# Optimization experiments

Measured on AMD Instinct MI355X. Metric: run time of the kernel, lower is better.

Reference implementation:

```python
import jax, jax.numpy as jnp
import numpy as np

B, T, D_MODEL, HEAD_DIM = 4, 4096, 2048, 128
NEG = -1e9  # matches torch's -1000000000.0 mask fill


def setup_inputs() -> dict:
    key = jax.random.key(0)
    ks = jax.random.split(key, 7)
    s = 0.02
    return {
        "x": jax.random.normal(ks[0], (B, T, D_MODEL), dtype=jnp.float32),
        "q_w": jax.random.normal(ks[1], (HEAD_DIM, D_MODEL), dtype=jnp.float32) * s,
        "q_b": jax.random.normal(ks[2], (HEAD_DIM,), dtype=jnp.float32) * s,
        "k_w": jax.random.normal(ks[3], (HEAD_DIM, D_MODEL), dtype=jnp.float32) * s,
        "k_b": jax.random.normal(ks[4], (HEAD_DIM,), dtype=jnp.float32) * s,
        "v_w": jax.random.normal(ks[5], (HEAD_DIM, D_MODEL), dtype=jnp.float32) * s,
        "v_b": jax.random.normal(ks[6], (HEAD_DIM,), dtype=jnp.float32) * s,
    }


def reference(x, q_w, q_b, k_w, k_b, v_w, v_b):
    # Linear projections: y = x @ W^T + b  -> [B, T, head_dim]
    q = jnp.einsum("btc,hc->bth", x, q_w) + q_b
    k = jnp.einsum("btc,hc->bth", x, k_w) + k_b
    v = jnp.einsum("btc,hc->bth", x, v_w) + v_b

    head_dim = q.shape[-1]
    # scores [B, T, T], scaled by 1/sqrt(head_dim)
    scores = jnp.einsum("bqh,bkh->bqk", q, k) / jnp.sqrt(jnp.float32(head_dim))
    # causal mask: additive -1e9 above the diagonal (future positions)
    t = scores.shape[-1]
    mask = jnp.triu(jnp.full((t, t), NEG, dtype=scores.dtype), k=1)
    scores = scores + mask
    probs = jax.nn.softmax(scores, axis=-1)
    # dropout p=0.0 -> identity (eval)
    y = jnp.einsum("bqk,bkh->bqh", probs, v)
    return y
```

## Files before the change

### kernel.cpp

```cpp
#include <hip/hip_runtime.h>

#define T_SEQ 4096
#define DMODEL 2048
#define HD 128

typedef float f32x4 __attribute__((ext_vector_type(4)));
typedef _Float16 f16x8 __attribute__((ext_vector_type(8)));

__device__ __forceinline__ unsigned short f2h(float f) {
  union { _Float16 h; unsigned short u; } v;
  v.h = (_Float16)f;
  return v.u;
}

__device__ __forceinline__ unsigned pk2h(float lo, float hi) {
  return (unsigned)f2h(lo) | ((unsigned)f2h(hi) << 16);
}

template <int CTRL>
__device__ __forceinline__ float dppmax(float x) {
  union { float f; int i; } a, b;
  a.f = x;
  b.i = __builtin_amdgcn_update_dpp(a.i, a.i, CTRL, 0xF, 0xF, false);
  return fmaxf(x, b.f);
}
template <int CTRL>
__device__ __forceinline__ float dppadd(float x) {
  union { float f; int i; } a, b;
  a.f = x;
  b.i = __builtin_amdgcn_update_dpp(a.i, a.i, CTRL, 0xF, 0xF, false);
  return x + b.f;
}
__device__ __forceinline__ float red16_max(float x) {
  x = dppmax<0xB1>(x); x = dppmax<0x4E>(x);
  x = dppmax<0x124>(x); x = dppmax<0x128>(x);
  return x;
}
__device__ __forceinline__ float red16_add(float x) {
  x = dppadd<0xB1>(x); x = dppadd<0x4E>(x);
  x = dppadd<0x124>(x); x = dppadd<0x128>(x);
  return x;
}

__global__ __launch_bounds__(256) void cvt_w_kernel(
    const float* __restrict__ qw, const float* __restrict__ qb,
    const float* __restrict__ kw, const float* __restrict__ kb,
    const float* __restrict__ vw, const float* __restrict__ vb,
    unsigned short* __restrict__ wb, float* __restrict__ biasc) {
  int idx = blockIdx.x * 256 + threadIdx.x;
  int e = idx * 4;
  int row = e >> 11;
  int col = e & 2047;
  const float* src = (row < 128) ? (qw + row * 2048)
                   : (row < 256) ? (kw + (row - 128) * 2048)
                                 : (vw + (row - 256) * 2048);
  float4 v = *(const float4*)(src + col);
  ushort4 o;
  o.x = f2h(v.x); o.y = f2h(v.y); o.z = f2h(v.z); o.w = f2h(v.w);
  *(ushort4*)(wb + e) = o;
  if (blockIdx.x == 0 && threadIdx.x < 384) {
    int n = threadIdx.x;
    biasc[n] = (n < 128) ? qb[n] : (n < 256) ? kb[n - 128] : vb[n - 256];
  }
}

#define SAB 40
__global__ __launch_bounds__(256, 3) void proj_kernel(
    const float* __restrict__ x, const unsigned short* __restrict__ wb,
    const float* __restrict__ biasc, unsigned short* __restrict__ qkv) {
  __shared__ unsigned short sA[64 * SAB];
  __shared__ unsigned short sB[128 * SAB];
  const int tid = threadIdx.x;
  const int lane = tid & 63;
  const int w = tid >> 6;
  const int fr = lane & 15;
  const int g = lane >> 4;
  const int m0 = blockIdx.x * 64;
  const int n0 = blockIdx.y * 128;
  const int wm = (w & 1) * 32;
  const int wn = (w >> 1) * 64;

  const int arow = tid >> 2;
  const int acolA = (tid & 3) * 8;
  const int brow = tid >> 1;
  const int bcolB = (tid & 1) * 16;
  const float* xp = x + (size_t)(m0 + arow) * DMODEL + acolA;
  const unsigned short* bp = wb + (size_t)(n0 + brow) * DMODEL + bcolB;

  f32x4 acc[2][4] = {};
  float4 ax0 = *(const float4*)(xp);
  float4 ax1 = *(const float4*)(xp + 4);
  uint4 bx0 = *(const uint4*)(bp);
  uint4 bx1 = *(const uint4*)(bp + 8);

  for (int k0 = 0; k0 < DMODEL; k0 += 32) {
    __syncthreads();
    uint4 pa;
    pa.x = pk2h(ax0.x, ax0.y); pa.y = pk2h(ax0.z, ax0.w);
    pa.z = pk2h(ax1.x, ax1.y); pa.w = pk2h(ax1.z, ax1.w);
    *(uint4*)&sA[arow * SAB + acolA] = pa;
    *(uint4*)&sB[brow * SAB + bcolB] = bx0;
    *(uint4*)&sB[brow * SAB + bcolB + 8] = bx1;
    __syncthreads();

    if (k0 + 32 < DMODEL) {
      ax0 = *(const float4*)(xp + k0 + 32);
      ax1 = *(const float4*)(xp + k0 + 36);
      bx0 = *(const uint4*)(bp + k0 + 32);
      bx1 = *(const uint4*)(bp + k0 + 40);
    }

    f16x8 af[2], bf[4];
#pragma unroll
    for (int i = 0; i < 2; ++i)
      af[i] = *(const f16x8*)&sA[(wm + 16 * i + fr) * SAB + g * 8];
#pragma unroll
    for (int jn = 0; jn < 4; ++jn)
      bf[jn] = *(const f16x8*)&sB[(wn + 16 * jn + fr) * SAB + g * 8];
#pragma unroll
    for (int i = 0; i < 2; ++i)
#pragma unroll
      for (int jn = 0; jn < 4; ++jn)
        acc[i][jn] = __builtin_amdgcn_mfma_f32_16x16x32_f16(af[i], bf[jn], acc[i][jn], 0, 0, 0);
  }

#pragma unroll
  for (int jn = 0; jn < 4; ++jn) {
    int n = n0 + wn + 16 * jn + fr;
    float bias = biasc[n];
#pragma unroll
    for (int i = 0; i < 2; ++i) {
      int mb = m0 + wm + 16 * i + g * 4;
#pragma unroll
      for (int r = 0; r < 4; ++r)
        qkv[(size_t)(mb + r) * 384 + n] = f2h(acc[i][jn][r] + bias);
    }
  }
}

#define SKS 136
#define SVS 72
#define SPS 72
__global__ __launch_bounds__(256, 3) void attn_kernel(
    const unsigned short* __restrict__ qkv, float* __restrict__ out,
    float* __restrict__ po, float* __restrict__ pml, int split) {
  __shared__ unsigned short sK[64 * SKS];
  __shared__ unsigned short sVt[128 * SVS];
  __shared__ unsigned short sP[64 * SPS];
  const int id = blockIdx.x;
  const int batch = blockIdx.y;
  int qt, c, nc;
  if (split) {
    if (id < 16)      { qt = id;                c = 0;          nc = 1; }
    else if (id < 48) { qt = 16 + ((id - 16) >> 1); c = (id - 16) & 1; nc = 2; }
    else if (id < 96) { qt = 32 + (id - 48) / 3;    c = (id - 48) % 3; nc = 3; }
    else              { qt = 48 + ((id - 96) >> 2); c = (id - 96) & 3; nc = 4; }
  } else { qt = id; c = 0; nc = 1; }
  const int qbase = qt * 64;
  const int t0 = c * 16;
  const int tend = min(t0 + 16, qt + 1);
  const int tid = threadIdx.x;
  const int lane = tid & 63;
  const int w = tid >> 6;
  const int fr = lane & 15;
  const int g = lane >> 4;
  const int va = tid >> 4;
  const int vu = tid & 15;
  const int vblk = ((va ^ (vu & 14)) << 2);
  const unsigned short* qkvb = qkv + (size_t)batch * T_SEQ * 384;

  f16x8 qf[4];
  {
    const unsigned short* qp = qkvb + (size_t)(qbase + 16 * w + fr) * 384 + g * 8;
#pragma unroll
    for (int s = 0; s < 4; ++s) qf[s] = *(const f16x8*)(qp + 32 * s);
  }
  f32x4 o[8] = {};
  float m_r[4], l_r[4];
#pragma unroll
  for (int r = 0; r < 4; ++r) { m_r[r] = -1e30f; l_r[r] = 0.f; }
  const float scale = 0.08838834764831845f;

  uint4 pk[4], pvv[4];
#pragma unroll
  for (int it = 0; it < 4; ++it) {
    int idx = it * 256 + tid;
    pk[it] = *(const uint4*)(qkvb + (size_t)(t0 * 64 + (idx >> 4)) * 384 + 128 + (idx & 15) * 8);
  }
#pragma unroll
  for (int i = 0; i < 4; ++i)
    pvv[i] = *(const uint4*)(qkvb + (size_t)(t0 * 64 + va + 16 * i) * 384 + 256 + vu * 8);

  for (int t = t0; t < tend; ++t) {
    const int kbase = t * 64;
    __syncthreads();
#pragma unroll
    for (int it = 0; it < 4; ++it) {
      int idx = it * 256 + tid;
      *(uint4*)&sK[(idx >> 4) * SKS + (idx & 15) * 8] = pk[it];
    }
    {
      const unsigned* w0 = (const unsigned*)&pvv[0];
      const unsigned* w1 = (const unsigned*)&pvv[1];
      const unsigned* w2 = (const unsigned*)&pvv[2];
      const unsigned* w3 = (const unsigned*)&pvv[3];
#pragma unroll
      for (int j2 = 0; j2 < 4; ++j2) {
        uint2 se, so;
        se.x = __builtin_amdgcn_perm(w1[j2], w0[j2], 0x05040100);
        se.y = __builtin_amdgcn_perm(w3[j2], w2[j2], 0x05040100);
        so.x = __builtin_amdgcn_perm(w1[j2], w0[j2], 0x07060302);
        so.y = __builtin_amdgcn_perm(w3[j2], w2[j2], 0x07060302);
        *(uint2*)&sVt[(8 * vu + 2 * j2) * SVS + vblk] = se;
        *(uint2*)&sVt[(8 * vu + 2 * j2 + 1) * SVS + vblk] = so;
      }
    }
    __syncthreads();

    if (t + 1 < tend) {
#pragma unroll
      for (int it = 0; it < 4; ++it) {
        int idx = it * 256 + tid;
        pk[it] = *(const uint4*)(qkvb + (size_t)((t + 1) * 64 + (idx >> 4)) * 384 + 128 + (idx & 15) * 8);
      }
#pragma unroll
      for (int i = 0; i < 4; ++i)
        pvv[i] = *(const uint4*)(qkvb + (size_t)((t + 1) * 64 + va + 16 * i) * 384 + 256 + vu * 8);
    }

    f32x4 sacc[4] = {};
#pragma unroll
    for (int ks = 0; ks < 4; ++ks)
#pragma unroll
      for (int tn = 0; tn < 4; ++tn) {
        f16x8 kf = *(const f16x8*)&sK[(16 * tn + fr) * SKS + 32 * ks + g * 8];
        sacc[tn] = __builtin_amdgcn_mfma_f32_16x16x32_f16(qf[ks], kf, sacc[tn], 0, 0, 0);
      }

    const bool diag = (t == qt);
    float pv[4][4];
#pragma unroll
    for (int r = 0; r < 4; ++r) {
      int grow = qbase + 16 * w + g * 4 + r;
      float mx = -1e30f;
#pragma unroll
      for (int tn = 0; tn < 4; ++tn) {
        float s = sacc[tn][r] * scale;
        if (diag && (kbase + 16 * tn + fr) > grow) s = -1e30f;
        pv[tn][r] = s;
        mx = fmaxf(mx, s);
      }
      mx = red16_max(mx);
      float mnew = fmaxf(m_r[r], mx);
      float alpha = __expf(m_r[r] - mnew);
      m_r[r] = mnew;
      float rs = 0.f;
#pragma unroll
      for (int tn = 0; tn < 4; ++tn) {
        float p = __expf(pv[tn][r] - mnew);
        pv[tn][r] = p;
        rs += p;
      }
      rs = red16_add(rs);
      l_r[r] = l_r[r] * alpha + rs;
#pragma unroll
      for (int nt = 0; nt < 8; ++nt) o[nt][r] *= alpha;
    }

#pragma unroll
    for (int r = 0; r < 4; ++r) {
      uint2 pw;
      pw.x = pk2h(pv[0][r], pv[1][r]);
      pw.y = pk2h(pv[2][r], pv[3][r]);
      *(uint2*)&sP[(16 * w + 4 * g + r) * SPS + 4 * fr] = pw;
    }

#pragma unroll
    for (int ks = 0; ks < 2; ++ks) {
      f16x8 pa = *(const f16x8*)&sP[(16 * w + fr) * SPS + 32 * ks + 8 * g];
#pragma unroll
      for (int nt = 0; nt < 8; ++nt) {
        int d = 16 * nt + fr;
        int blk = ((8 * ks + 2 * g) ^ ((d >> 3) & 14)) << 1;
        f16x8 vf = *(const f16x8*)&sVt[d * SVS + (blk << 1)];
        o[nt] = __builtin_amdgcn_mfma_f32_16x16x32_f16(pa, vf, o[nt], 0, 0, 0);
      }
    }
  }

  if (nc == 1) {
#pragma unroll
    for (int r = 0; r < 4; ++r) {
      float inv = 1.0f / l_r[r];
      int grow = qbase + 16 * w + g * 4 + r;
      float* op = out + ((size_t)batch * T_SEQ + grow) * HD;
#pragma unroll
      for (int nt = 0; nt < 8; ++nt)
        op[16 * nt + fr] = o[nt][r] * inv;
    }
  } else {
    size_t slot = ((size_t)batch * 160 + id) * 64;
#pragma unroll
    for (int r = 0; r < 4; ++r) {
      int lrow = 16 * w + g * 4 + r;
      float* op = po + (slot + lrow) * 128;
#pragma unroll
      for (int nt = 0; nt < 8; ++nt)
        op[16 * nt + fr] = o[nt][r];
      if (fr == 0) {
        pml[(slot + lrow) * 2] = m_r[r];
        pml[(slot + lrow) * 2 + 1] = l_r[r];
      }
    }
  }
}

__global__ __launch_bounds__(256) void combine_kernel(
    const float* __restrict__ po, const float* __restrict__ pml,
    float* __restrict__ out) {
  int gr = blockIdx.x * 2 + (threadIdx.x >> 7);
  int d = threadIdx.x & 127;
  int batch = gr / 3072;
  int ridx = gr - batch * 3072;
  int qt = 16 + (ridx >> 6);
  int rr = ridx & 63;
  int nc = 1 + (qt >> 4);
  int sb = (qt < 32) ? 16 + (qt - 16) * 2
         : (qt < 48) ? 48 + (qt - 32) * 3
                     : 96 + (qt - 48) * 4;
  size_t base = ((size_t)batch * 160 + sb) * 64 + rr;
  float mi[4], li[4];
  float M = -1e30f;
#pragma unroll
  for (int i = 0; i < 4; ++i) {
    if (i < nc) {
      mi[i] = pml[(base + (size_t)i * 64) * 2];
      li[i] = pml[(base + (size_t)i * 64) * 2 + 1];
      M = fmaxf(M, mi[i]);
    }
  }
  float L = 0.f, acc = 0.f;
#pragma unroll
  for (int i = 0; i < 4; ++i) {
    if (i < nc) {
      float sc = __expf(mi[i] - M);
      L += li[i] * sc;
      acc += po[(base + (size_t)i * 64) * 128 + d] * sc;
    }
  }
  out[((size_t)batch * T_SEQ + qt * 64 + rr) * HD + d] = acc / L;
}

extern "C" void kernel_launch(void* const* d_in, const int* in_sizes, int n_in,
                              void* d_out, int out_size, void* d_ws, size_t ws_size,
                              hipStream_t stream) {
  const float* x  = (const float*)d_in[0];
  const float* qw = (const float*)d_in[1];
  const float* qb = (const float*)d_in[2];
  const float* kw = (const float*)d_in[3];
  const float* kb = (const float*)d_in[4];
  const float* vw = (const float*)d_in[5];
  const float* vb = (const float*)d_in[6];
  float* out = (float*)d_out;

  unsigned short* qkv = (unsigned short*)d_ws;
  unsigned short* wb  = qkv + (size_t)16384 * 384;
  float* biasc = (float*)(wb + (size_t)384 * 2048);
  float* po  = (float*)((char*)d_ws + 14157312);
  float* pml = po + (size_t)640 * 64 * 128;
  size_t need = 14157312 + (size_t)640 * 64 * 128 * 4 + (size_t)640 * 64 * 2 * 4;
  int split = (ws_size >= need) ? 1 : 0;

  cvt_w_kernel<<<768, 256, 0, stream>>>(qw, qb, kw, kb, vw, vb, wb, biasc);
  proj_kernel<<<dim3(256, 3), 256, 0, stream>>>(x, wb, biasc, qkv);
  attn_kernel<<<dim3(split ? 160 : 64, 4), 256, 0, stream>>>(qkv, out, po, pml, split);
  if (split)
    combine_kernel<<<6144, 256, 0, stream>>>(po, pml, out);
}
```

Baseline: 144.0 us.

## Halve projection and attention tile sizes to 32 rows for more blocks

The projection GEMM tile shrinks from 64x128 to 32x128 and its grid doubles. Attention query and key tiles shrink from 64 to 32 rows with 128-thread blocks, and the KV-split schedule is rebalanced so chunks split the tile count evenly. The combine indexing and workspace layout are updated to match. The aim is to raise occupancy and balance causal work across CUs, at the cost of less data reuse per tile and more K/V reloads.

```diff
diff --git a/kernel.cpp b/kernel.cpp
--- a/kernel.cpp
+++ b/kernel.cpp
@@ -65,100 +65,97 @@
 }
 
 #define SAB 40
-__global__ __launch_bounds__(256, 3) void proj_kernel(
+__global__ __launch_bounds__(256, 4) void proj_kernel(
     const float* __restrict__ x, const unsigned short* __restrict__ wb,
     const float* __restrict__ biasc, unsigned short* __restrict__ qkv) {
-  __shared__ unsigned short sA[64 * SAB];
+  __shared__ unsigned short sA[32 * SAB];
   __shared__ unsigned short sB[128 * SAB];
   const int tid = threadIdx.x;
   const int lane = tid & 63;
   const int w = tid >> 6;
   const int fr = lane & 15;
   const int g = lane >> 4;
-  const int m0 = blockIdx.x * 64;
+  const int m0 = blockIdx.x * 32;
   const int n0 = blockIdx.y * 128;
-  const int wm = (w & 1) * 32;
-  const int wn = (w >> 1) * 64;
-
-  const int arow = tid >> 2;
-  const int acolA = (tid & 3) * 8;
+  const int wn = w * 32;
+
+  const int arow = tid >> 3;
+  const int acol = (tid & 7) * 4;
   const int brow = tid >> 1;
-  const int bcolB = (tid & 1) * 16;
-  const float* xp = x + (size_t)(m0 + arow) * DMODEL + acolA;
-  const unsigned short* bp = wb + (size_t)(n0 + brow) * DMODEL + bcolB;
-
-  f32x4 acc[2][4] = {};
-  float4 ax0 = *(const float4*)(xp);
-  float4 ax1 = *(const float4*)(xp + 4);
+  const int bcol = (tid & 1) * 16;
+  const float* xp = x + (size_t)(m0 + arow) * DMODEL + acol;
+  const unsigned short* bp = wb + (size_t)(n0 + brow) * DMODEL + bcol;
+
+  f32x4 acc[2][2] = {};
+  float4 ax = *(const float4*)(xp);
   uint4 bx0 = *(const uint4*)(bp);
   uint4 bx1 = *(const uint4*)(bp + 8);
 
   for (int k0 = 0; k0 < DMODEL; k0 += 32) {
     __syncthreads();
-    uint4 pa;
-    pa.x = pk2h(ax0.x, ax0.y); pa.y = pk2h(ax0.z, ax0.w);
-    pa.z = pk2h(ax1.x, ax1.y); pa.w = pk2h(ax1.z, ax1.w);
-    *(uint4*)&sA[arow * SAB + acolA] = pa;
-    *(uint4*)&sB[brow * SAB + bcolB] = bx0;
-    *(uint4*)&sB[brow * SAB + bcolB + 8] = bx1;
+    uint2 pa;
+    pa.x = pk2h(ax.x, ax.y); pa.y = pk2h(ax.z, ax.w);
+    *(uint2*)&sA[arow * SAB + acol] = pa;
+    *(uint4*)&sB[brow * SAB + bcol] = bx0;
+    *(uint4*)&sB[brow * SAB + bcol + 8] = bx1;
     __syncthreads();
 
     if (k0 + 32 < DMODEL) {
-      ax0 = *(const float4*)(xp + k0 + 32);
-      ax1 = *(const float4*)(xp + k0 + 36);
+      ax  = *(const float4*)(xp + k0 + 32);
       bx0 = *(const uint4*)(bp + k0 + 32);
       bx1 = *(const uint4*)(bp + k0 + 40);
     }
 
-    f16x8 af[2], bf[4];
+    f16x8 af[2], bf[2];
 #pragma unroll
     for (int i = 0; i < 2; ++i)
-      af[i] = *(const f16x8*)&sA[(wm + 16 * i + fr) * SAB + g * 8];
-#pragma unroll
-    for (int jn = 0; jn < 4; ++jn)
-      bf[jn] = *(const f16x8*)&sB[(wn + 16 * jn + fr) * SAB + g * 8];
+      af[i] = *(const f16x8*)&sA[(16 * i + fr) * SAB + g * 8];
+#pragma unroll
+    for (int j = 0; j < 2; ++j)
+      bf[j] = *(const f16x8*)&sB[(wn + 16 * j + fr) * SAB + g * 8];
 #pragma unroll
     for (int i = 0; i < 2; ++i)
 #pragma unroll
-      for (int jn = 0; jn < 4; ++jn)
-        acc[i][jn] = __builtin_amdgcn_mfma_f32_16x16x32_f16(af[i], bf[jn], acc[i][jn], 0, 0, 0);
-  }
-
-#pragma unroll
-  for (int jn = 0; jn < 4; ++jn) {
-    int n = n0 + wn + 16 * jn + fr;
+      for (int j = 0; j < 2; ++j)
+        acc[i][j] = __builtin_amdgcn_mfma_f32_16x16x32_f16(af[i], bf[j], acc[i][j], 0, 0, 0);
+  }
+
+#pragma unroll
+  for (int j = 0; j < 2; ++j) {
+    int n = n0 + wn + 16 * j + fr;
     float bias = biasc[n];
 #pragma unroll
     for (int i = 0; i < 2; ++i) {
-      int mb = m0 + wm + 16 * i + g * 4;
+      int mb = m0 + 16 * i + g * 4;
 #pragma unroll
       for (int r = 0; r < 4; ++r)
-        qkv[(size_t)(mb + r) * 384 + n] = f2h(acc[i][jn][r] + bias);
+        qkv[(size_t)(mb + r) * 384 + n] = f2h(acc[i][j][r] + bias);
     }
   }
 }
 
 #define SKS 136
-#define SVS 72
-#define SPS 72
-__global__ __launch_bounds__(256, 3) void attn_kernel(
+#define SVS 40
+#define SPS 40
+__global__ __launch_bounds__(128, 3) void attn_kernel(
     const unsigned short* __restrict__ qkv, float* __restrict__ out,
     float* __restrict__ po, float* __restrict__ pml, int split) {
-  __shared__ unsigned short sK[64 * SKS];
+  __shared__ unsigned short sK[32 * SKS];
   __shared__ unsigned short sVt[128 * SVS];
-  __shared__ unsigned short sP[64 * SPS];
+  __shared__ unsigned short sP[32 * SPS];
   const int id = blockIdx.x;
   const int batch = blockIdx.y;
   int qt, c, nc;
   if (split) {
-    if (id < 16)      { qt = id;                c = 0;          nc = 1; }
-    else if (id < 48) { qt = 16 + ((id - 16) >> 1); c = (id - 16) & 1; nc = 2; }
-    else if (id < 96) { qt = 32 + (id - 48) / 3;    c = (id - 48) % 3; nc = 3; }
-    else              { qt = 48 + ((id - 96) >> 2); c = (id - 96) & 3; nc = 4; }
+    if (id < 32)       { qt = id;                   c = 0;             nc = 1; }
+    else if (id < 96)  { qt = 32 + ((id - 32) >> 1); c = (id - 32) & 1; nc = 2; }
+    else if (id < 192) { qt = 64 + (id - 96) / 3;    c = (id - 96) % 3; nc = 3; }
+    else               { qt = 96 + ((id - 192) >> 2); c = (id - 192) & 3; nc = 4; }
   } else { qt = id; c = 0; nc = 1; }
-  const int qbase = qt * 64;
-  const int t0 = c * 16;
-  const int tend = min(t0 + 16, qt + 1);
+  const int qbase = qt * 32;
+  const int ntiles = qt + 1;
+  const int t0 = (c * ntiles) / nc;
+  const int tend = ((c + 1) * ntiles) / nc;
   const int tid = threadIdx.x;
   const int lane = tid & 63;
   const int w = tid >> 6;
@@ -166,7 +163,7 @@
   const int g = lane >> 4;
   const int va = tid >> 4;
   const int vu = tid & 15;
-  const int vblk = ((va ^ (vu & 14)) << 2);
+  const int vblk = (va ^ (vu & 6)) * 4;
   const unsigned short* qkvb = qkv + (size_t)batch * T_SEQ * 384;
 
   f16x8 qf[4];
@@ -184,19 +181,21 @@
   uint4 pk[4], pvv[4];
 #pragma unroll
   for (int it = 0; it < 4; ++it) {
-    int idx = it * 256 + tid;
-    pk[it] = *(const uint4*)(qkvb + (size_t)(t0 * 64 + (idx >> 4)) * 384 + 128 + (idx & 15) * 8);
-  }
-#pragma unroll
-  for (int i = 0; i < 4; ++i)
-    pvv[i] = *(const uint4*)(qkvb + (size_t)(t0 * 64 + va + 16 * i) * 384 + 256 + vu * 8);
+    int idx = it * 128 + tid;
+    pk[it] = *(const uint4*)(qkvb + (size_t)(t0 * 32 + (idx >> 4)) * 384 + 128 + (idx & 15) * 8);
+  }
+#pragma unroll
+  for (int i = 0; i < 4; ++i) {
+    int rv = 2 * va + 16 * (i & 1) + (i >> 1);
+    pvv[i] = *(const uint4*)(qkvb + (size_t)(t0 * 32 + rv) * 384 + 256 + vu * 8);
+  }
 
   for (int t = t0; t < tend; ++t) {
-    const int kbase = t * 64;
+    const int kbase = t * 32;
     __syncthreads();
 #pragma unroll
     for (int it = 0; it < 4; ++it) {
-      int idx = it * 256 + tid;
+      int idx = it * 128 + tid;
       *(uint4*)&sK[(idx >> 4) * SKS + (idx & 15) * 8] = pk[it];
     }
     {
@@ -220,31 +219,33 @@
     if (t + 1 < tend) {
 #pragma unroll
       for (int it = 0; it < 4; ++it) {
-        int idx = it * 256 + tid;
-        pk[it] = *(const uint4*)(qkvb + (size_t)((t + 1) * 64 + (idx >> 4)) * 384 + 128 + (idx & 15) * 8);
-      }
-#pragma unroll
-      for (int i = 0; i < 4; ++i)
-        pvv[i] = *(const uint4*)(qkvb + (size_t)((t + 1) * 64 + va + 16 * i) * 384 + 256 + vu * 8);
-    }
-
-    f32x4 sacc[4] = {};
+        int idx = it * 128 + tid;
+        pk[it] = *(const uint4*)(qkvb + (size_t)((t + 1) * 32 + (idx >> 4)) * 384 + 128 + (idx & 15) * 8);
+      }
+#pragma unroll
+      for (int i = 0; i < 4; ++i) {
+        int rv = 2 * va + 16 * (i & 1) + (i >> 1);
+        pvv[i] = *(const uint4*)(qkvb + (size_t)((t + 1) * 32 + rv) * 384 + 256 + vu * 8);
+      }
+    }
+
+    f32x4 sacc[2] = {};
 #pragma unroll
     for (int ks = 0; ks < 4; ++ks)
 #pragma unroll
-      for (int tn = 0; tn < 4; ++tn) {
+      for (int tn = 0; tn < 2; ++tn) {
         f16x8 kf = *(const f16x8*)&sK[(16 * tn + fr) * SKS + 32 * ks + g * 8];
         sacc[tn] = __builtin_amdgcn_mfma_f32_16x16x32_f16(qf[ks], kf, sacc[tn], 0, 0, 0);
       }
 
     const bool diag = (t == qt);
-    float pv[4][4];
+    float pv[2][4];
 #pragma unroll
     for (int r = 0; r < 4; ++r) {
       int grow = qbase + 16 * w + g * 4 + r;
       float mx = -1e30f;
 #pragma unroll
-      for (int tn = 0; tn < 4; ++tn) {
+      for (int tn = 0; tn < 2; ++tn) {
         float s = sacc[tn][r] * scale;
         if (diag && (kbase + 16 * tn + fr) > grow) s = -1e30f;
         pv[tn][r] = s;
@@ -256,7 +257,7 @@
       m_r[r] = mnew;
       float rs = 0.f;
 #pragma unroll
-      for (int tn = 0; tn < 4; ++tn) {
+      for (int tn = 0; tn < 2; ++tn) {
         float p = __expf(pv[tn][r] - mnew);
         pv[tn][r] = p;
         rs += p;
@@ -268,21 +269,16 @@
     }
 
 #pragma unroll
-    for (int r = 0; r < 4; ++r) {
-      uint2 pw;
-      pw.x = pk2h(pv[0][r], pv[1][r]);
-      pw.y = pk2h(pv[2][r], pv[3][r]);
-      *(uint2*)&sP[(16 * w + 4 * g + r) * SPS + 4 * fr] = pw;
-    }
-
-#pragma unroll
-    for (int ks = 0; ks < 2; ++ks) {
-      f16x8 pa = *(const f16x8*)&sP[(16 * w + fr) * SPS + 32 * ks + 8 * g];
+    for (int r = 0; r < 4; ++r)
+      *(unsigned*)&sP[(16 * w + 4 * g + r) * SPS + 2 * fr] = pk2h(pv[0][r], pv[1][r]);
+
+    {
+      f16x8 pa = *(const f16x8*)&sP[(16 * w + fr) * SPS + 8 * g];
 #pragma unroll
       for (int nt = 0; nt < 8; ++nt) {
         int d = 16 * nt + fr;
-        int blk = ((8 * ks + 2 * g) ^ ((d >> 3) & 14)) << 1;
-        f16x8 vf = *(const f16x8*)&sVt[d * SVS + (blk << 1)];
+        int blk = (2 * g) ^ ((d >> 3) & 6);
+        f16x8 vf = *(const f16x8*)&sVt[d * SVS + blk * 4];
         o[nt] = __builtin_amdgcn_mfma_f32_16x16x32_f16(pa, vf, o[nt], 0, 0, 0);
       }
     }
@@ -299,7 +295,7 @@
         op[16 * nt + fr] = o[nt][r] * inv;
     }
   } else {
-    size_t slot = ((size_t)batch * 160 + id) * 64;
+    size_t slot = ((size_t)batch * 320 + id) * 32;
 #pragma unroll
     for (int r = 0; r < 4; ++r) {
       int lrow = 16 * w + g * 4 + r;
@@ -322,20 +318,20 @@
   int d = threadIdx.x & 127;
   int batch = gr / 3072;
   int ridx = gr - batch * 3072;
-  int qt = 16 + (ridx >> 6);
-  int rr = ridx & 63;
-  int nc = 1 + (qt >> 4);
-  int sb = (qt < 32) ? 16 + (qt - 16) * 2
-         : (qt < 48) ? 48 + (qt - 32) * 3
-                     : 96 + (qt - 48) * 4;
-  size_t base = ((size_t)batch * 160 + sb) * 64 + rr;
+  int qt = 32 + (ridx >> 5);
+  int rr = ridx & 31;
+  int nc = 1 + (qt >> 5);
+  int sb = (qt < 64) ? 32 + (qt - 32) * 2
+         : (qt < 96) ? 96 + (qt - 64) * 3
+                     : 192 + (qt - 96) * 4;
+  size_t base = ((size_t)batch * 320 + sb) * 32 + rr;
   float mi[4], li[4];
   float M = -1e30f;
 #pragma unroll
   for (int i = 0; i < 4; ++i) {
     if (i < nc) {
-      mi[i] = pml[(base + (size_t)i * 64) * 2];
-      li[i] = pml[(base + (size_t)i * 64) * 2 + 1];
+      mi[i] = pml[(base + (size_t)i * 32) * 2];
+      li[i] = pml[(base + (size_t)i * 32) * 2 + 1];
       M = fmaxf(M, mi[i]);
     }
   }
@@ -345,10 +341,10 @@
     if (i < nc) {
       float sc = __expf(mi[i] - M);
       L += li[i] * sc;
-      acc += po[(base + (size_t)i * 64) * 128 + d] * sc;
-    }
-  }
-  out[((size_t)batch * T_SEQ + qt * 64 + rr) * HD + d] = acc / L;
+      acc += po[(base + (size_t)i * 32) * 128 + d] * sc;
+    }
+  }
+  out[((size_t)batch * T_SEQ + qt * 32 + rr) * HD + d] = acc / L;
 }
 
 extern "C" void kernel_launch(void* const* d_in, const int* in_sizes, int n_in,
@@ -367,13 +363,13 @@
   unsigned short* wb  = qkv + (size_t)16384 * 384;
   float* biasc = (float*)(wb + (size_t)384 * 2048);
   float* po  = (float*)((char*)d_ws + 14157312);
-  float* pml = po + (size_t)640 * 64 * 128;
-  size_t need = 14157312 + (size_t)640 * 64 * 128 * 4 + (size_t)640 * 64 * 2 * 4;
+  float* pml = po + (size_t)1280 * 32 * 128;
+  size_t need = 14157312 + (size_t)1280 * 32 * 128 * 4 + (size_t)1280 * 32 * 2 * 4;
   int split = (ws_size >= need) ? 1 : 0;
 
   cvt_w_kernel<<<768, 256, 0, stream>>>(qw, qb, kw, kb, vw, vb, wb, biasc);
-  proj_kernel<<<dim3(256, 3), 256, 0, stream>>>(x, wb, biasc, qkv);
-  attn_kernel<<<dim3(split ? 160 : 64, 4), 256, 0, stream>>>(qkv, out, po, pml, split);
+  proj_kernel<<<dim3(512, 3), 256, 0, stream>>>(x, wb, biasc, qkv);
+  attn_kernel<<<dim3(split ? 320 : 128, 4), 128, 0, stream>>>(qkv, out, po, pml, split);
   if (split)
     combine_kernel<<<6144, 256, 0, stream>>>(po, pml, out);
 }
```

After: 215.3 us. 1.5x slower.

## Balance causal split chunks, double-stage K tile, add MFMA priority and lazy rescale

Applied to the files above, without the earlier changes.

Key tiles are now divided evenly across the split chunks of each query tile, replacing fixed 16-tile chunks that left the last chunk short. The K tile for the next step is written to shared memory after the score phase and its global prefetch runs two steps ahead, moving the barriers so K staging overlaps the P·V MFMAs. s_setprio is raised around the MFMA loops. The running-max rescale of o and l is skipped when the row maximum does not increase. The extra barrier placement and the divergent rescale branch add some risk but keep the same maths.

```diff
diff --git a/kernel.cpp b/kernel.cpp
--- a/kernel.cpp
+++ b/kernel.cpp
@@ -157,8 +157,9 @@
     else              { qt = 48 + ((id - 96) >> 2); c = (id - 96) & 3; nc = 4; }
   } else { qt = id; c = 0; nc = 1; }
   const int qbase = qt * 64;
-  const int t0 = c * 16;
-  const int tend = min(t0 + 16, qt + 1);
+  const int ntl = qt + 1;
+  const int t0 = (c * ntl) / nc;
+  const int tend = ((c + 1) * ntl) / nc;
   const int tid = threadIdx.x;
   const int lane = tid & 63;
   const int w = tid >> 6;
@@ -190,15 +191,23 @@
 #pragma unroll
   for (int i = 0; i < 4; ++i)
     pvv[i] = *(const uint4*)(qkvb + (size_t)(t0 * 64 + va + 16 * i) * 384 + 256 + vu * 8);
+#pragma unroll
+  for (int it = 0; it < 4; ++it) {
+    int idx = it * 256 + tid;
+    *(uint4*)&sK[(idx >> 4) * SKS + (idx & 15) * 8] = pk[it];
+  }
+  if (t0 + 1 < tend) {
+#pragma unroll
+    for (int it = 0; it < 4; ++it) {
+      int idx = it * 256 + tid;
+      pk[it] = *(const uint4*)(qkvb + (size_t)((t0 + 1) * 64 + (idx >> 4)) * 384 + 128 + (idx & 15) * 8);
+    }
+  }
+  __syncthreads();
 
   for (int t = t0; t < tend; ++t) {
     const int kbase = t * 64;
-    __syncthreads();
-#pragma unroll
-    for (int it = 0; it < 4; ++it) {
-      int idx = it * 256 + tid;
-      *(uint4*)&sK[(idx >> 4) * SKS + (idx & 15) * 8] = pk[it];
-    }
+
     {
       const unsigned* w0 = (const unsigned*)&pvv[0];
       const unsigned* w1 = (const unsigned*)&pvv[1];
@@ -215,20 +224,14 @@
         *(uint2*)&sVt[(8 * vu + 2 * j2 + 1) * SVS + vblk] = so;
       }
     }
-    __syncthreads();
-
     if (t + 1 < tend) {
-#pragma unroll
-      for (int it = 0; it < 4; ++it) {
-        int idx = it * 256 + tid;
-        pk[it] = *(const uint4*)(qkvb + (size_t)((t + 1) * 64 + (idx >> 4)) * 384 + 128 + (idx & 15) * 8);
-      }
 #pragma unroll
       for (int i = 0; i < 4; ++i)
         pvv[i] = *(const uint4*)(qkvb + (size_t)((t + 1) * 64 + va + 16 * i) * 384 + 256 + vu * 8);
     }
 
     f32x4 sacc[4] = {};
+    __builtin_amdgcn_s_setprio(1);
 #pragma unroll
     for (int ks = 0; ks < 4; ++ks)
 #pragma unroll
@@ -236,6 +239,7 @@
         f16x8 kf = *(const f16x8*)&sK[(16 * tn + fr) * SKS + 32 * ks + g * 8];
         sacc[tn] = __builtin_amdgcn_mfma_f32_16x16x32_f16(qf[ks], kf, sacc[tn], 0, 0, 0);
       }
+    __builtin_amdgcn_s_setprio(0);
 
     const bool diag = (t == qt);
     float pv[4][4];
@@ -251,20 +255,22 @@
         mx = fmaxf(mx, s);
       }
       mx = red16_max(mx);
-      float mnew = fmaxf(m_r[r], mx);
-      float alpha = __expf(m_r[r] - mnew);
-      m_r[r] = mnew;
+      if (mx > m_r[r]) {
+        float alpha = __expf(m_r[r] - mx);
+        m_r[r] = mx;
+        l_r[r] *= alpha;
+#pragma unroll
+        for (int nt = 0; nt < 8; ++nt) o[nt][r] *= alpha;
+      }
       float rs = 0.f;
 #pragma unroll
       for (int tn = 0; tn < 4; ++tn) {
-        float p = __expf(pv[tn][r] - mnew);
+        float p = __expf(pv[tn][r] - m_r[r]);
         pv[tn][r] = p;
         rs += p;
       }
       rs = red16_add(rs);
-      l_r[r] = l_r[r] * alpha + rs;
-#pragma unroll
-      for (int nt = 0; nt < 8; ++nt) o[nt][r] *= alpha;
+      l_r[r] += rs;
     }
 
 #pragma unroll
@@ -274,18 +280,36 @@
       pw.y = pk2h(pv[2][r], pv[3][r]);
       *(uint2*)&sP[(16 * w + 4 * g + r) * SPS + 4 * fr] = pw;
     }
-
+    __syncthreads();
+
+    if (t + 1 < tend) {
+#pragma unroll
+      for (int it = 0; it < 4; ++it) {
+        int idx = it * 256 + tid;
+        *(uint4*)&sK[(idx >> 4) * SKS + (idx & 15) * 8] = pk[it];
+      }
+      if (t + 2 < tend) {
+#pragma unroll
+        for (int it = 0; it < 4; ++it) {
+          int idx = it * 256 + tid;
+          pk[it] = *(const uint4*)(qkvb + (size_t)((t + 2) * 64 + (idx >> 4)) * 384 + 128 + (idx & 15) * 8);
+        }
+      }
+    }
+    __builtin_amdgcn_s_setprio(1);
 #pragma unroll
     for (int ks = 0; ks < 2; ++ks) {
       f16x8 pa = *(const f16x8*)&sP[(16 * w + fr) * SPS + 32 * ks + 8 * g];
 #pragma unroll
       for (int nt = 0; nt < 8; ++nt) {
         int d = 16 * nt + fr;
-        int blk = ((8 * ks + 2 * g) ^ ((d >> 3) & 14)) << 1;
-        f16x8 vf = *(const f16x8*)&sVt[d * SVS + (blk << 1)];
+        int blk = ((8 * ks + 2 * g) ^ ((d >> 3) & 14)) << 2;
+        f16x8 vf = *(const f16x8*)&sVt[d * SVS + blk];
         o[nt] = __builtin_amdgcn_mfma_f32_16x16x32_f16(pa, vf, o[nt], 0, 0, 0);
       }
     }
+    __builtin_amdgcn_s_setprio(0);
+    __syncthreads();
   }
 
   if (nc == 1) {
```

After: 227.2 us. +57.8%, slower.
